# Kernel optimization log

Hardware: AMD Instinct MI355X
Metric: run time of the kernel (lower is better)

## Reference

```python
import jax, jax.numpy as jnp
import numpy as np

B, CIN, COUT, H, W = 16, 128, 128, 64, 64
E, PS, FF = 8, 16, 8
GC, HID, HC = 4 * FF, 64, COUT * 4  # gate_channel, gate hidden, bottleneck hidden


def conv(x, w, stride=1, pad=0, groups=1):
    # x: [B,C,H,W], w: [O,I/groups,kh,kw]
    return jax.lax.conv_general_dilated(
        x, w, (stride, stride), [(pad, pad), (pad, pad)], feature_group_count=groups)


def group_norm(x, scale, bias, groups, eps=1e-5):
    b, c = x.shape[:2]
    xr = x.reshape(b, groups, c // groups, *x.shape[2:])
    m = xr.mean(axis=(2, 3, 4), keepdims=True)
    v = xr.var(axis=(2, 3, 4), keepdims=True)
    xr = (xr - m) * jax.lax.rsqrt(v + eps)
    return xr.reshape(x.shape) * scale[None, :, None, None] + bias[None, :, None, None]


def setup_inputs() -> dict:
    key = jax.random.key(0)
    ks = jax.random.split(key, 8)
    f = lambda k, shp: jax.random.normal(k, shp, jnp.float32) * 0.05
    return dict(
        x=jax.random.normal(ks[0], (B, CIN, H, W), jnp.float32),
        w_exp=f(ks[1], (E, COUT, CIN, 3, 3)),
        gn_exp_s=jnp.ones((E, COUT), jnp.float32),
        gn_exp_b=jnp.zeros((E, COUT), jnp.float32),
        w1=f(ks[2], (GC, HID)), b1=jnp.zeros((HID,), jnp.float32),
        w2=f(ks[3], (HID, E)), b2=jnp.zeros((E,), jnp.float32),
        w_pw1=f(ks[4], (HC, COUT, 1, 1)),
        gn1_s=jnp.ones((HC,), jnp.float32), gn1_b=jnp.zeros((HC,), jnp.float32),
        w_dw=f(ks[5], (HC, 1, 3, 3)),
        gn2_s=jnp.ones((HC,), jnp.float32), gn2_b=jnp.zeros((HC,), jnp.float32),
        w_pw2=f(ks[6], (COUT, HC, 1, 1)),
        gn3_s=jnp.ones((COUT,), jnp.float32), gn3_b=jnp.zeros((COUT,), jnp.float32),
    )


def reference(x, w_exp, gn_exp_s, gn_exp_b, w1, b1, w2, b2,
              w_pw1, gn1_s, gn1_b, w_dw, gn2_s, gn2_b, w_pw2, gn3_s, gn3_b):
    # ---- Conv experts (residual 3x3 conv + GN + SiLU), vmapped over experts ----
    def expert(w, s, b):
        y = conv(x, w, pad=1)
        y = group_norm(y, s, b, groups=min(8, COUT))
        return jax.nn.silu(y) + x  # use_residual=True, CIN == COUT

    ys = jax.vmap(expert)(w_exp, gn_exp_s, gn_exp_b)  # [E,B,C,H,W]

    # ---- Router gate: Fourier features of patch-center coordinates ----
    ph, pw = H // PS, W // PS
    cy = (jnp.arange(ph, dtype=jnp.float32) + 0.5) / ph
    cx = (jnp.arange(pw, dtype=jnp.float32) + 0.5) / pw
    freqs = (2.0 ** jnp.arange(FF, dtype=jnp.float32)) * jnp.pi
    ay = cy[:, None] * freqs  # [ph,FF]
    ax = cx[:, None] * freqs  # [pw,FF]
    feats = jnp.concatenate([
        jnp.broadcast_to(jnp.sin(ay)[:, None, :], (ph, pw, FF)),
        jnp.broadcast_to(jnp.cos(ay)[:, None, :], (ph, pw, FF)),
        jnp.broadcast_to(jnp.sin(ax)[None, :, :], (ph, pw, FF)),
        jnp.broadcast_to(jnp.cos(ax)[None, :, :], (ph, pw, FF)),
    ], axis=-1)  # [ph,pw,4*FF] == gate_channel
    hgate = jax.nn.silu(feats @ w1 + b1)
    wts = jax.nn.softmax(hgate @ w2 + b2, axis=-1)  # [ph,pw,E]

    # ---- Patch-wise combine of expert outputs ----
    wmap = jnp.repeat(jnp.repeat(wts, PS, axis=0), PS, axis=1)  # [H,W,E]
    combined = jnp.einsum('ebchw,hwe->bchw', ys, wmap)

    # ---- Inverted bottleneck: 1x1 -> dw3x3 -> 1x1(stride2) with GN+SiLU ----
    h = jax.nn.silu(group_norm(conv(combined, w_pw1), gn1_s, gn1_b, groups=8))
    h = jax.nn.silu(group_norm(conv(h, w_dw, pad=1, groups=HC), gn2_s, gn2_b, groups=8))
    h = jax.nn.silu(group_norm(conv(h, w_pw2, stride=2), gn3_s, gn3_b, groups=8))
    return h  # [B, COUT, H//2, W//2]
```

## Files before the change

### kernel.cpp

```cpp
#include <hip/hip_runtime.h>
#include <hip/hip_bf16.h>


#define B_ 16
#define CIN_ 128
#define COUT_ 128
#define H_ 64
#define W_ 64
#define HW_ 4096
#define E_ 8
#define FF_ 8
#define GC_ 32
#define HID_ 64
#define HC_ 512

typedef __hip_bfloat16 bf16;
typedef __bf16 bf16x8 __attribute__((ext_vector_type(8)));
typedef float f32x4 __attribute__((ext_vector_type(4)));
typedef float f32x16 __attribute__((ext_vector_type(16)));

__device__ __forceinline__ float siluf(float v) {
  return v * __builtin_amdgcn_rcpf(1.f + __expf(-v));
}
__device__ __forceinline__ float bf2f(bf16 v) { return __bfloat162float(v); }
__device__ __forceinline__ bf16 f2bf(float v) { return __float2bfloat16(v); }

__device__ __forceinline__ void async16(void* lds, const void* g) {
  __builtin_amdgcn_global_load_lds(
      (const __attribute__((address_space(1))) unsigned int*)g,
      (__attribute__((address_space(3))) unsigned int*)lds, 16, 0, 0);
}

__global__ __launch_bounds__(256) void prep_kernel(
    const float* __restrict__ x, bf16* __restrict__ xT,
    const float* __restrict__ w_exp, bf16* __restrict__ wT,
    const float* __restrict__ w_pw1, const float* __restrict__ w_pw2,
    bf16* __restrict__ wp1T, bf16* __restrict__ wp2T,
    const float* __restrict__ w1, const float* __restrict__ b1,
    const float* __restrict__ w2, const float* __restrict__ b2,
    float* __restrict__ wts) {
  __shared__ float t[128][65];
  int blk = blockIdx.x;
  int tid = threadIdx.x;

  if (blk < 1024) {
    int b = blk >> 6, h = blk & 63;
    int w = tid & 63, c4 = tid >> 6;
    const float* xb = x + ((size_t)(b * 128) * 64 + h) * 64;
#pragma unroll 4
    for (int rep = 0; rep < 32; ++rep) {
      int ci = rep * 4 + c4;
      t[ci][w] = xb[(size_t)ci * HW_ + w];
    }
    __syncthreads();
    bf16* dst = xT + (size_t)(b * 64 + h) * 8192;
#pragma unroll 4
    for (int rep = 0; rep < 32; ++rep) {
      int o = rep * 256 + tid;
      int cg = o >> 9, w2 = (o >> 3) & 63, lo = o & 7;
      dst[o] = f2bf(t[cg * 8 + lo][w2]);
    }
  } else if (blk < 5632) {
    int idx = (blk - 1024) * 256 + tid;
    if (idx < 1179648) {
      int lo = idx & 7;
      int co = (idx >> 3) & 127;
      int cg = (idx >> 10) & 15;
      int rest = idx >> 14;
      int tap = rest % 9, e = rest / 9;
      int ci = cg * 8 + lo;
      wT[idx] = f2bf(w_exp[(((size_t)(e * 128 + co) * 128 + ci) * 9) + tap]);
    }
  } else if (blk < 6144) {
    int idx = (blk - 5632) * 256 + tid;
    if (idx < 65536) wp1T[idx] = f2bf(w_pw1[idx]);
    else wp2T[idx - 65536] = f2bf(w_pw2[idx - 65536]);
  } else {
    int p = tid;
    if (p >= 16) return;
    int i = p >> 2, j = p & 3;
    float cy = (i + 0.5f) * 0.25f;
    float cx = (j + 0.5f) * 0.25f;
    float feats[GC_];
#pragma unroll
    for (int f = 0; f < FF_; ++f) {
      float fr = 3.14159265358979f * (float)(1 << f);
      float ay = cy * fr, ax = cx * fr;
      feats[f] = sinf(ay);
      feats[FF_ + f] = cosf(ay);
      feats[2 * FF_ + f] = sinf(ax);
      feats[3 * FF_ + f] = cosf(ax);
    }
    float hid[HID_];
    for (int k = 0; k < HID_; ++k) {
      float a = b1[k];
#pragma unroll
      for (int m = 0; m < GC_; ++m) a = fmaf(feats[m], w1[m * HID_ + k], a);
      hid[k] = siluf(a);
    }
    float lg[E_];
    float mx = -1e30f;
#pragma unroll
    for (int e = 0; e < E_; ++e) {
      float a = b2[e];
      for (int k = 0; k < HID_; ++k) a = fmaf(hid[k], w2[k * E_ + e], a);
      lg[e] = a;
      mx = fmaxf(mx, a);
    }
    float s = 0.f;
#pragma unroll
    for (int e = 0; e < E_; ++e) { lg[e] = __expf(lg[e] - mx); s += lg[e]; }
    float inv = 1.f / s;
#pragma unroll
    for (int e = 0; e < E_; ++e) wts[p * E_ + e] = lg[e] * inv;
  }
}

__global__ __launch_bounds__(256, 2) void conv_mfma(
    const bf16* __restrict__ xT, const bf16* __restrict__ wT,
    float* __restrict__ statsE, bf16* __restrict__ ys) {
  __shared__ __align__(16) char xls[4 * 6336];
  __shared__ __align__(16) char wls[2][3 * 8192];
  __shared__ float red[4][8][2];

  int blk = blockIdx.x;
  int xcd = blk & 7;
  int r2 = blk >> 3;
  int b = xcd * 2 + (r2 & 1);
  int rest = r2 >> 1;
  int rt = rest & 15, e = rest >> 4;

  int tid = threadIdx.x, lane = tid & 63, wave = tid >> 6;
  int hi = lane >> 5, l31 = lane & 31;
  int h0 = rt * 4;

  if (tid < 48) {
    int cg = tid / 12, rem = tid % 12;
    int r = rem >> 1, edge = rem & 1;
    *(uint4*)(xls + cg * 6336 + r * 1056 + edge * 1040) = make_uint4(0u, 0u, 0u, 0u);
  }
  int rbad = (rt == 0) ? 0 : (rt == 15 ? 5 : -1);
  if (rbad >= 0) {
    int cg = tid >> 6, slot = (tid & 63) + 1;
    *(uint4*)(xls + cg * 6336 + rbad * 1056 + slot * 16) = make_uint4(0u, 0u, 0u, 0u);
  }

  f32x16 acc[4][2];
#pragma unroll
  for (int mt = 0; mt < 4; ++mt)
#pragma unroll
    for (int nt = 0; nt < 2; ++nt)
#pragma unroll
      for (int r = 0; r < 16; ++r) acc[mt][nt][r] = 0.f;

  for (int q = 0; q < 4; ++q) {
    if (q) __syncthreads();
    {
      int cg = wave;
#pragma unroll
      for (int r = 0; r < 6; ++r) {
        int h = h0 - 1 + r;
        if ((unsigned)h < 64u) {
          const char* g = (const char*)xT +
              ((size_t)((b * 64 + h) * 16) + q * 4 + cg) * 1024 + lane * 16;
          async16(xls + cg * 6336 + r * 1056 + 16, g);
        }
      }
    }
#pragma unroll
    for (int s = 0; s < 6; ++s) {
      int seg = wave * 6 + s;
      int tap = seg >> 3, rem = seg & 7;
      int cg = rem >> 1, cb = rem & 1;
      const char* g = (const char*)wT +
          ((size_t)(((e * 9 + tap) * 16) + q * 4 + cg) * 128 + cb * 64) * 16 + lane * 16;
      async16(wls[0] + (tap * 4 + cg) * 2048 + cb * 1024, g);
    }
    __syncthreads();

    for (int dr = 0; dr < 3; ++dr) {
      int buf = dr & 1;
      if (dr < 2) {
#pragma unroll
        for (int s = 0; s < 6; ++s) {
          int seg = wave * 6 + s;
          int tap = seg >> 3, rem = seg & 7;
          int cg = rem >> 1, cb = rem & 1;
          const char* g = (const char*)wT +
              ((size_t)(((e * 9 + (dr + 1) * 3 + tap) * 16) + q * 4 + cg) * 128 + cb * 64) * 16 +
              lane * 16;
          async16(wls[buf ^ 1] + (tap * 4 + cg) * 2048 + cb * 1024, g);
        }
      }
      int r_local = wave + dr;
      const char* wb = wls[buf];
      const char* xrow = xls;
      bf16x8 afp[2][2], bfp[2][2];
      {
        int cgl = hi;
        afp[0][0] = *(const bf16x8*)(wb + cgl * 2048 + (0 * 32 + l31) * 16);
        afp[0][1] = *(const bf16x8*)(wb + cgl * 2048 + (1 * 32 + l31) * 16);
        const char* xr = xrow + cgl * 6336 + r_local * 1056;
        bfp[0][0] = *(const bf16x8*)(xr + (0 * 32 + l31 + 0) * 16);
        bfp[0][1] = *(const bf16x8*)(xr + (1 * 32 + l31 + 0) * 16);
      }
#pragma unroll
      for (int s = 0; s < 12; ++s) {
        int mh = s & 1;
        int cura = s & 1, curb = (s >> 1) & 1;
        if (s < 11) {
          int s1 = s + 1;
          int ds1 = s1 >> 2, ks1 = (s1 >> 1) & 1, mh1 = s1 & 1;
          int cgl1 = ks1 * 2 + hi;
          const char* wt1 = wb + ds1 * 8192 + cgl1 * 2048;
          afp[s1 & 1][0] = *(const bf16x8*)(wt1 + ((mh1 * 2 + 0) * 32 + l31) * 16);
          afp[s1 & 1][1] = *(const bf16x8*)(wt1 + ((mh1 * 2 + 1) * 32 + l31) * 16);
          if (mh1 == 0) {
            const char* xr1 = xrow + cgl1 * 6336 + r_local * 1056;
            bfp[(s1 >> 1) & 1][0] = *(const bf16x8*)(xr1 + (0 * 32 + l31 + ds1) * 16);
            bfp[(s1 >> 1) & 1][1] = *(const bf16x8*)(xr1 + (1 * 32 + l31 + ds1) * 16);
          }
        }
#pragma unroll
        for (int i = 0; i < 2; ++i)
#pragma unroll
          for (int nt = 0; nt < 2; ++nt)
            acc[mh * 2 + i][nt] = __builtin_amdgcn_mfma_f32_32x32x16_bf16(
                afp[cura][i], bfp[curb][nt], acc[mh * 2 + i][nt], 0, 0, 0);
      }
      if (dr < 2) __syncthreads();
    }
  }

  int hh = h0 + wave;
  bf16* yb = ys + (size_t)((e * 16 + b) * 128) * 4096;
#pragma unroll
  for (int mt = 0; mt < 4; ++mt) {
    float s0 = 0.f, ss0 = 0.f, s1 = 0.f, ss1 = 0.f;
#pragma unroll
    for (int nt = 0; nt < 2; ++nt) {
      int w = nt * 32 + l31;
      int pos = hh * 64 + w;
#pragma unroll
      for (int r = 0; r < 16; ++r) {
        float v = acc[mt][nt][r];
        if (r < 8) { s0 += v; ss0 += v * v; } else { s1 += v; ss1 += v * v; }
        int row = (r & 3) + 8 * (r >> 2) + 4 * hi;
        yb[(size_t)(mt * 32 + row) * 4096 + pos] = f2bf(v);
      }
    }
#pragma unroll
    for (int off = 32; off; off >>= 1) {
      s0 += __shfl_down(s0, off, 64);
      ss0 += __shfl_down(ss0, off, 64);
      s1 += __shfl_down(s1, off, 64);
      ss1 += __shfl_down(ss1, off, 64);
    }
    if (lane == 0) {
      red[wave][mt * 2][0] = s0; red[wave][mt * 2][1] = ss0;
      red[wave][mt * 2 + 1][0] = s1; red[wave][mt * 2 + 1][1] = ss1;
    }
  }
  __syncthreads();
  if (tid < 16) {
    int g = tid >> 1, which = tid & 1;
    float t = red[0][g][which] + red[1][g][which] + red[2][g][which] + red[3][g][which];
    atomicAdd(&statsE[((e * 16 + b) * 8 + g) * 2 + which], t);
  }
}

__global__ __launch_bounds__(256) void combine_cl(
    const float* __restrict__ x, const bf16* __restrict__ ys,
    const float* __restrict__ stE, const float* __restrict__ gns,
    const float* __restrict__ gnb, const float* __restrict__ wts,
    bf16* __restrict__ ccl) {
  __shared__ bf16 tile[64][132];
  int blk = blockIdx.x;
  int xcd = blk & 7;
  int k2 = blk >> 3;
  int b = xcd * 2 + (k2 >> 6);
  int h = k2 & 63;
  int t = threadIdx.x;
  int oct = t & 7, cq = t >> 3;
  int w0 = oct * 8;
  int gidx = cq >> 2;
  int pid = (h >> 4) * 4 + (w0 >> 4);
  int pos = h * 64 + w0;

  float m_[8], r_[8], wt_[8];
#pragma unroll
  for (int e = 0; e < 8; ++e) {
    float S = stE[((e * 16 + b) * 8 + gidx) * 2];
    float SS = stE[((e * 16 + b) * 8 + gidx) * 2 + 1];
    float mean = S * (1.f / 65536.f);
    float var = SS * (1.f / 65536.f) - mean * mean;
    m_[e] = mean;
    r_[e] = rsqrtf(var + 1e-5f);
    wt_[e] = wts[pid * 8 + e];
  }

#pragma unroll
  for (int k = 0; k < 4; ++k) {
    int co = cq * 4 + k;
    const float* xp = x + ((size_t)(b * 128 + co) << 12) + pos;
    float v[8];
    float4 xa = *(const float4*)xp;
    float4 xb2 = *(const float4*)(xp + 4);
    v[0] = xa.x; v[1] = xa.y; v[2] = xa.z; v[3] = xa.w;
    v[4] = xb2.x; v[5] = xb2.y; v[6] = xb2.z; v[7] = xb2.w;
#pragma unroll
    for (int e = 0; e < 8; ++e) {
      uint4 u = *(const uint4*)(ys + ((size_t)((e * 16 + b) * 128 + co) << 12) + pos);
      const bf16* pv = (const bf16*)&u;
      float sc = r_[e] * gns[e * 128 + co];
      float sh = gnb[e * 128 + co] - m_[e] * sc;
#pragma unroll
      for (int j = 0; j < 8; ++j) {
        float yn = bf2f(pv[j]) * sc + sh;
        v[j] = fmaf(siluf(yn), wt_[e], v[j]);
      }
    }
#pragma unroll
    for (int j = 0; j < 8; ++j) tile[w0 + j][co] = f2bf(v[j]);
  }
  __syncthreads();
  int row = t >> 2, q = t & 3;
  char* dst = (char*)ccl + ((size_t)(b * 4096 + h * 64 + row)) * 256 + q * 64;
  const char* src = (const char*)&tile[row][0] + q * 64;
#pragma unroll
  for (int i = 0; i < 4; ++i)
    *(uint4*)(dst + i * 16) = *(const uint4*)(src + i * 16);
}

__global__ __launch_bounds__(256) void pw1_mfma(
    const bf16* __restrict__ ccl, const bf16* __restrict__ wp1T,
    bf16* __restrict__ h1cl, float* __restrict__ stats1) {
  __shared__ __align__(16) char bls[32768];
  __shared__ __align__(16) char ls2[34816];
  __shared__ float red[4][2][2];
  int blk = blockIdx.x;
  int n0 = blk * 128;
  int t = threadIdx.x, lane = t & 63, wave = t >> 6;
  int quad = lane >> 4, l15 = lane & 15;
  int b = n0 >> 12;

#pragma unroll
  for (int i = 0; i < 8; ++i) {
    int id = t + 256 * i;
    int r = id >> 4, c = id & 15;
    *(uint4*)(bls + c * 2048 + r * 16) =
        *(const uint4*)((const char*)ccl + (size_t)(n0 + r) * 256 + c * 16);
  }

  for (int mtile = 0; mtile < 4; ++mtile) {
    int m0 = mtile * 128;
    char* als = ls2;
#pragma unroll
    for (int i = 0; i < 8; ++i) {
      int id = t + 256 * i;
      int r = id >> 4, c = id & 15;
      *(uint4*)(als + c * 2048 + r * 16) =
          *(const uint4*)((const char*)wp1T + (size_t)(m0 + r) * 256 + c * 16);
    }
    __syncthreads();

    f32x4 acc[8][2];
#pragma unroll
    for (int mt = 0; mt < 8; ++mt)
#pragma unroll
      for (int nt = 0; nt < 2; ++nt) acc[mt][nt] = (f32x4){0.f, 0.f, 0.f, 0.f};

#pragma unroll
    for (int kc = 0; kc < 4; ++kc) {
      int cgq = kc * 4 + quad;
      bf16x8 af[8];
#pragma unroll
      for (int mt = 0; mt < 8; ++mt)
        af[mt] = *(const bf16x8*)(als + cgq * 2048 + (mt * 16 + l15) * 16);
      bf16x8 bfr[2];
#pragma unroll
      for (int nt = 0; nt < 2; ++nt)
        bfr[nt] = *(const bf16x8*)(bls + cgq * 2048 + (wave * 32 + nt * 16 + l15) * 16);
#pragma unroll
      for (int mt = 0; mt < 8; ++mt)
#pragma unroll
        for (int nt = 0; nt < 2; ++nt)
          acc[mt][nt] = __builtin_amdgcn_mfma_f32_16x16x32_bf16(
              af[mt], bfr[nt], acc[mt][nt], 0, 0, 0);
    }

    __syncthreads();
    float s[2] = {0.f, 0.f}, ss[2] = {0.f, 0.f};
    bf16* tile = (bf16*)ls2;
#pragma unroll
    for (int mt = 0; mt < 8; ++mt) {
      int gi = mt >> 2;
#pragma unroll
      for (int nt = 0; nt < 2; ++nt) {
        int n = wave * 32 + nt * 16 + l15;
#pragma unroll
        for (int r = 0; r < 4; ++r) {
          float v = acc[mt][nt][r];
          s[gi] += v;
          ss[gi] += v * v;
          tile[n * 132 + mt * 16 + quad * 4 + r] = f2bf(v);
        }
      }
    }
#pragma unroll
    for (int gi = 0; gi < 2; ++gi) {
#pragma unroll
      for (int off = 32; off; off >>= 1) {
        s[gi] += __shfl_down(s[gi], off, 64);
        ss[gi] += __shfl_down(ss[gi], off, 64);
      }
    }
    if (lane == 0) {
      red[wave][0][0] = s[0]; red[wave][0][1] = ss[0];
      red[wave][1][0] = s[1]; red[wave][1][1] = ss[1];
    }
    __syncthreads();
    if (t < 4) {
      int gi = t >> 1, which = t & 1;
      float v = red[0][gi][which] + red[1][gi][which] + red[2][gi][which] + red[3][gi][which];
      atomicAdd(&stats1[(b * 8 + mtile * 2 + gi) * 2 + which], v);
    }
#pragma unroll
    for (int i = 0; i < 8; ++i) {
      int id = t + 256 * i;
      int r = id >> 4, q = id & 15;
      char* dst = (char*)h1cl + (size_t)(n0 + r) * 1024 + m0 * 2 + q * 16;
      const char* src = (const char*)tile + r * 264 + q * 16;
      *(uint4*)dst = *(const uint4*)src;
    }
    __syncthreads();
  }
}

__global__ __launch_bounds__(256) void dw_cl(
    const bf16* __restrict__ h1cl, const float* __restrict__ w_dw,
    const float* __restrict__ st1, const float* __restrict__ gs,
    const float* __restrict__ gb, bf16* __restrict__ h2cl,
    float* __restrict__ stats2) {
  __shared__ __align__(16) bf16 tile[18 * 66 * 16];
  __shared__ float red2[4][2];
  int blk = blockIdx.x;
  int ht = blk & 3, hcg = (blk >> 2) & 31, b = blk >> 7;
  int h0 = ht * 16;
  int hc0 = hcg * 16;
  int hcb = hcg >> 2;
  int t = threadIdx.x;

  float S1 = st1[(b * 8 + hcb) * 2], SS1 = st1[(b * 8 + hcb) * 2 + 1];
  float mean = S1 * (1.f / 262144.f);
  float var1 = SS1 * (1.f / 262144.f) - mean * mean;
  float rstd = rsqrtf(var1 + 1e-5f);
  float scale[16], shift[16];
#pragma unroll
  for (int j = 0; j < 16; ++j) {
    float g = gs[hc0 + j];
    scale[j] = rstd * g;
    shift[j] = gb[hc0 + j] - mean * rstd * g;
  }

  for (int i = 0; i < 5; ++i) {
    int idx = t + 256 * i;
    if (idx >= 1188) break;
    int row = idx / 66, wslot = idx - row * 66;
    int hh = h0 - 1 + row;
    int w = wslot - 1;
    int swz = (wslot >> 2) & 3;
    bf16* dst = tile + (row * 66 + wslot) * 16;
    if ((unsigned)hh < 64u && (unsigned)w < 64u) {
      const char* p = (const char*)h1cl + ((size_t)(b * 4096 + hh * 64 + w) * 512 + hc0) * 2;
      uint4 a0 = *(const uint4*)p;
      uint4 a1 = *(const uint4*)(p + 16);
      const bf16* pv = (const bf16*)&a0;
      const bf16* pv1 = (const bf16*)&a1;
      bf16 outv[16];
#pragma unroll
      for (int j = 0; j < 8; ++j)
        outv[j] = f2bf(siluf(bf2f(pv[j]) * scale[j] + shift[j]));
#pragma unroll
      for (int j = 0; j < 8; ++j)
        outv[8 + j] = f2bf(siluf(bf2f(pv1[j]) * scale[8 + j] + shift[8 + j]));
#pragma unroll
      for (int qq = 0; qq < 4; ++qq) {
        int ph = (qq + swz) & 3;
        *(uint2*)(dst + ph * 4) = *(const uint2*)(outv + qq * 4);
      }
    } else {
      *(uint4*)dst = make_uint4(0u, 0u, 0u, 0u);
      *(uint4*)(dst + 8) = make_uint4(0u, 0u, 0u, 0u);
    }
  }
  __syncthreads();

  int w = t & 63, q = t >> 6;
  float wv[9][4];
#pragma unroll
  for (int j = 0; j < 4; ++j) {
    int hc = hc0 + q * 4 + j;
#pragma unroll
    for (int tap = 0; tap < 9; ++tap) wv[tap][j] = w_dw[hc * 9 + tap];
  }

  f32x4 win[3][3];
  float acc_s = 0.f, acc_ss = 0.f;

  auto ld4 = [&](int r, int dwi) -> f32x4 {
    int slot = w + dwi;
    int ph = (q + (slot >> 2)) & 3;
    const bf16* p = tile + (r * 66 + slot) * 16 + ph * 4;
    uint2 u = *(const uint2*)p;
    const bf16* pb = (const bf16*)&u;
    return (f32x4){bf2f(pb[0]), bf2f(pb[1]), bf2f(pb[2]), bf2f(pb[3])};
  };

#pragma unroll
  for (int dwi = 0; dwi < 3; ++dwi) {
    win[0][dwi] = ld4(0, dwi);
    win[1][dwi] = ld4(1, dwi);
  }
#pragma unroll
  for (int orow = 0; orow < 16; ++orow) {
    int rnew = orow + 2;
    int ringn = rnew % 3;
#pragma unroll
    for (int dwi = 0; dwi < 3; ++dwi) win[ringn][dwi] = ld4(rnew, dwi);
    f32x4 acc = (f32x4){0.f, 0.f, 0.f, 0.f};
#pragma unroll
    for (int dr = 0; dr < 3; ++dr) {
      int ring = (orow + dr) % 3;
#pragma unroll
      for (int dwi = 0; dwi < 3; ++dwi) {
#pragma unroll
        for (int j = 0; j < 4; ++j)
          acc[j] = fmaf(win[ring][dwi][j], wv[dr * 3 + dwi][j], acc[j]);
      }
    }
#pragma unroll
    for (int j = 0; j < 4; ++j) { acc_s += acc[j]; acc_ss += acc[j] * acc[j]; }
    if (!(orow & 1) && !(w & 1)) {
      int hglob = h0 + orow;
      int pos2 = (hglob >> 1) * 32 + (w >> 1);
      bf16 tmp[4];
#pragma unroll
      for (int j = 0; j < 4; ++j) tmp[j] = f2bf(acc[j]);
      *(uint2*)((char*)h2cl + ((size_t)(b * 1024 + pos2) * 512 + hc0 + q * 4) * 2) =
          *(const uint2*)tmp;
    }
  }

#pragma unroll
  for (int off = 32; off; off >>= 1) {
    acc_s += __shfl_down(acc_s, off, 64);
    acc_ss += __shfl_down(acc_ss, off, 64);
  }
  int wave = t >> 6;
  if ((t & 63) == 0) { red2[wave][0] = acc_s; red2[wave][1] = acc_ss; }
  __syncthreads();
  if (t < 2) {
    float v = red2[0][t] + red2[1][t] + red2[2][t] + red2[3][t];
    atomicAdd(&stats2[(b * 8 + hcb) * 2 + t], v);
  }
}

__global__ __launch_bounds__(256) void pw2_mfma(
    const bf16* __restrict__ h2, const bf16* __restrict__ wp2T,
    const float* __restrict__ st2, const float* __restrict__ gs2,
    const float* __restrict__ gb2, float* __restrict__ h3,
    float* __restrict__ stats3) {
  __shared__ __align__(16) char als[2][8192];
  __shared__ __align__(16) char bls[2][4096];
  __shared__ float red[4][8][2];
  int blk = blockIdx.x;
  int n0 = blk * 64;
  int b = n0 >> 10, posb = n0 & 1023;
  int t = threadIdx.x, lane = t & 63, wave = t >> 6;
  int quad = lane >> 4, l15 = lane & 15;
  int wbase = wave * 16;
  int c4 = t >> 6, r = t & 63;

  auto load_bls = [&](char* dst, int kc) {
    int hc0 = (kc * 4 + c4) * 8;
    int g = hc0 >> 6;
    float S = st2[(b * 8 + g) * 2], SS = st2[(b * 8 + g) * 2 + 1];
    float mean = S * (1.f / 262144.f);
    float rstd = rsqrtf(SS * (1.f / 262144.f) - mean * mean + 1e-5f);
    uint4 u = *(const uint4*)((const char*)h2 + (size_t)(n0 + r) * 1024 +
                              (size_t)(kc * 4 + c4) * 16);
    const bf16* pv = (const bf16*)&u;
    bf16 outv[8];
#pragma unroll
    for (int j = 0; j < 8; ++j) {
      float xv = bf2f(pv[j]);
      xv = (xv - mean) * rstd * gs2[hc0 + j] + gb2[hc0 + j];
      outv[j] = f2bf(siluf(xv));
    }
    *(uint4*)dst = *(const uint4*)outv;
  };

  f32x4 acc[8];
#pragma unroll
  for (int mt = 0; mt < 8; ++mt) acc[mt] = (f32x4){0.f, 0.f, 0.f, 0.f};

  {
#pragma unroll
    for (int i = 0; i < 2; ++i) {
      int id = t + 256 * i;
      int cc = id >> 7, rr = id & 127;
      *(uint4*)(als[0] + cc * 2048 + rr * 16) =
          *(const uint4*)((const char*)wp2T + (size_t)rr * 1024 + cc * 16);
    }
    load_bls(bls[0] + c4 * 1024 + r * 16, 0);
  }
#pragma unroll
  for (int kc = 0; kc < 16; ++kc) {
    __syncthreads();
    if (kc + 1 < 16) {
      int nb = (kc + 1) & 1;
#pragma unroll
      for (int i = 0; i < 2; ++i) {
        int id = t + 256 * i;
        int cc = id >> 7, rr = id & 127;
        *(uint4*)(als[nb] + cc * 2048 + rr * 16) =
            *(const uint4*)((const char*)wp2T + (size_t)rr * 1024 + ((kc + 1) * 4 + cc) * 16);
      }
      load_bls(bls[nb] + c4 * 1024 + r * 16, kc + 1);
    }
    int buf = kc & 1;
    bf16x8 bf1 = *(const bf16x8*)(bls[buf] + quad * 1024 + (wbase + l15) * 16);
#pragma unroll
    for (int mt = 0; mt < 8; ++mt) {
      bf16x8 af = *(const bf16x8*)(als[buf] + quad * 2048 + (mt * 16 + l15) * 16);
      acc[mt] = __builtin_amdgcn_mfma_f32_16x16x32_bf16(af, bf1, acc[mt], 0, 0, 0);
    }
  }

#pragma unroll
  for (int mt = 0; mt < 8; ++mt) {
    float s = 0.f, ss = 0.f;
    int pos = posb + wbase + l15;
#pragma unroll
    for (int rr = 0; rr < 4; ++rr) {
      float v = acc[mt][rr];
      s += v;
      ss += v * v;
      int co = mt * 16 + quad * 4 + rr;
      h3[(size_t)(b * 128 + co) * 1024 + pos] = v;
    }
#pragma unroll
    for (int off = 32; off; off >>= 1) {
      s += __shfl_down(s, off, 64);
      ss += __shfl_down(ss, off, 64);
    }
    if (lane == 0) { red[wave][mt][0] = s; red[wave][mt][1] = ss; }
  }
  __syncthreads();
  if (t < 16) {
    int mt = t >> 1, which = t & 1;
    float v = red[0][mt][which] + red[1][mt][which] + red[2][mt][which] + red[3][mt][which];
    atomicAdd(&stats3[(b * 8 + mt) * 2 + which], v);
  }
}

__global__ void out_kernel(const float* __restrict__ h3, const float* __restrict__ stats,
                           const float* __restrict__ gs, const float* __restrict__ gb,
                           float* __restrict__ out) {
  const int total4 = (B_ * COUT_ * 1024) >> 2;
  for (int i4 = blockIdx.x * blockDim.x + threadIdx.x; i4 < total4;
       i4 += gridDim.x * blockDim.x) {
    int idx = i4 << 2;
    int c = (idx >> 10) & 127;
    int b = idx >> 17;
    int bg = b * 8 + (c >> 4);
    float S = stats[bg * 2], SS = stats[bg * 2 + 1];
    float mean = S * (1.f / 16384.f);
    float var = SS * (1.f / 16384.f) - mean * mean;
    float rstd = rsqrtf(var + 1e-5f);
    float sc = rstd * gs[c];
    float sh = gb[c] - mean * sc;
    float4 hv = *(const float4*)(h3 + idx);
    float4 res;
    res.x = siluf(hv.x * sc + sh);
    res.y = siluf(hv.y * sc + sh);
    res.z = siluf(hv.z * sc + sh);
    res.w = siluf(hv.w * sc + sh);
    *(float4*)(out + idx) = res;
  }
}

extern "C" void kernel_launch(void* const* d_in, const int* in_sizes, int n_in,
                              void* d_out, int out_size, void* d_ws, size_t ws_size,
                              hipStream_t stream) {
  const float* x = (const float*)d_in[0];
  const float* w_exp = (const float*)d_in[1];
  const float* gn_exp_s = (const float*)d_in[2];
  const float* gn_exp_b = (const float*)d_in[3];
  const float* w1 = (const float*)d_in[4];
  const float* b1 = (const float*)d_in[5];
  const float* w2 = (const float*)d_in[6];
  const float* b2 = (const float*)d_in[7];
  const float* w_pw1 = (const float*)d_in[8];
  const float* gn1_s = (const float*)d_in[9];
  const float* gn1_b = (const float*)d_in[10];
  const float* w_dw = (const float*)d_in[11];
  const float* gn2_s = (const float*)d_in[12];
  const float* gn2_b = (const float*)d_in[13];
  const float* w_pw2 = (const float*)d_in[14];
  const float* gn3_s = (const float*)d_in[15];
  const float* gn3_b = (const float*)d_in[16];

  char* ws = (char*)d_ws;
  const size_t WP1T_OFF = 16384;
  const size_t WP2T_OFF = WP1T_OFF + 131072;
  const size_t XT_OFF = WP2T_OFF + 131072;
  const size_t WT_OFF = XT_OFF + 16777216;
  const size_t YS_OFF = WT_OFF + 2359296;
  const size_t NEEDED = YS_OFF + 134217728;
  if (ws_size < NEEDED) return;

  float* wts = (float*)ws;
  float* stats1 = (float*)(ws + 1024);
  float* stats2 = (float*)(ws + 2048);
  float* stats3 = (float*)(ws + 3072);
  float* statsE = (float*)(ws + 4096);
  bf16* wp1T = (bf16*)(ws + WP1T_OFF);
  bf16* wp2T = (bf16*)(ws + WP2T_OFF);
  bf16* xT = (bf16*)(ws + XT_OFF);
  bf16* ccl = (bf16*)(ws + XT_OFF);
  bf16* wT = (bf16*)(ws + WT_OFF);
  bf16* ys = (bf16*)(ws + YS_OFF);
  bf16* h1cl = (bf16*)(ws + YS_OFF);
  bf16* h2cl = (bf16*)(ws + YS_OFF + 67108864);
  float* h3 = (float*)(ws + YS_OFF + 83886080);

  hipMemsetAsync(ws, 0, 16384, stream);
  prep_kernel<<<6145, 256, 0, stream>>>(x, xT, w_exp, wT, w_pw1, w_pw2, wp1T, wp2T,
                                        w1, b1, w2, b2, wts);
  conv_mfma<<<E_ * B_ * 16, 256, 0, stream>>>(xT, wT, statsE, ys);
  combine_cl<<<B_ * 64, 256, 0, stream>>>(x, ys, statsE, gn_exp_s, gn_exp_b, wts, ccl);
  pw1_mfma<<<512, 256, 0, stream>>>(ccl, wp1T, h1cl, stats1);
  dw_cl<<<B_ * 32 * 4, 256, 0, stream>>>(h1cl, w_dw, stats1, gn1_s, gn1_b, h2cl, stats2);
  pw2_mfma<<<256, 256, 0, stream>>>(h2cl, wp2T, stats2, gn2_s, gn2_b, h3, stats3);
  out_kernel<<<1024, 256, 0, stream>>>(h3, stats3, gn3_s, gn3_b, (float*)d_out);
}
```

Before: 437.6 us.

## Split conv and pw2 launches, fold stats memset into prep kernel

Removes the hipMemsetAsync by zeroing the stats region inside prep_kernel's last block. Splits the expert conv launch into two launches of four experts each via an e_base offset. Splits pw2_mfma over output-channel halves, doubling the grid to 512 blocks with half the accumulators and smaller LDS per block. The pw2 split gains occupancy and parallelism but recomputes the GN2+SiLU B-tile in both halves. The conv split adds a launch boundary with no clear benefit.

New measurement: 432.9 us. About the same (-1.1%).

```diff
diff --git a/kernel.cpp b/kernel.cpp
--- a/kernel.cpp
+++ b/kernel.cpp
@@ -76,6 +76,8 @@
     if (idx < 65536) wp1T[idx] = f2bf(w_pw1[idx]);
     else wp2T[idx - 65536] = f2bf(w_pw2[idx - 65536]);
   } else {
+    uint4* z = (uint4*)((char*)wts + 1024);
+    for (int i = tid; i < 960; i += 256) z[i] = make_uint4(0u, 0u, 0u, 0u);
     int p = tid;
     if (p >= 16) return;
     int i = p >> 2, j = p & 3;
@@ -118,7 +120,7 @@
 
 __global__ __launch_bounds__(256, 2) void conv_mfma(
     const bf16* __restrict__ xT, const bf16* __restrict__ wT,
-    float* __restrict__ statsE, bf16* __restrict__ ys) {
+    float* __restrict__ statsE, bf16* __restrict__ ys, int e_base) {
   __shared__ __align__(16) char xls[4 * 6336];
   __shared__ __align__(16) char wls[2][3 * 8192];
   __shared__ float red[4][8][2];
@@ -128,7 +130,7 @@
   int r2 = blk >> 3;
   int b = xcd * 2 + (r2 & 1);
   int rest = r2 >> 1;
-  int rt = rest & 15, e = rest >> 4;
+  int rt = rest & 15, e = e_base + (rest >> 4);
 
   int tid = threadIdx.x, lane = tid & 63, wave = tid >> 6;
   int hi = lane >> 5, l31 = lane & 31;
@@ -571,11 +573,14 @@
     const float* __restrict__ st2, const float* __restrict__ gs2,
     const float* __restrict__ gb2, float* __restrict__ h3,
     float* __restrict__ stats3) {
-  __shared__ __align__(16) char als[2][8192];
+  __shared__ __align__(16) char als[2][4096];
   __shared__ __align__(16) char bls[2][4096];
-  __shared__ float red[4][8][2];
+  __shared__ float red[4][4][2];
   int blk = blockIdx.x;
-  int n0 = blk * 64;
+  int mhalf = blk >> 8;
+  int nblk = blk & 255;
+  int n0 = nblk * 64;
+  int m0 = mhalf * 64;
   int b = n0 >> 10, posb = n0 & 1023;
   int t = threadIdx.x, lane = t & 63, wave = t >> 6;
   int quad = lane >> 4, l15 = lane & 15;
@@ -600,19 +605,18 @@
     }
     *(uint4*)dst = *(const uint4*)outv;
   };
-
-  f32x4 acc[8];
-#pragma unroll
-  for (int mt = 0; mt < 8; ++mt) acc[mt] = (f32x4){0.f, 0.f, 0.f, 0.f};
+  auto load_als = [&](char* dstbase, int kc) {
+    *(uint4*)(dstbase + c4 * 1024 + r * 16) =
+        *(const uint4*)((const char*)wp2T + (size_t)(m0 + r) * 1024 +
+                        (size_t)(kc * 4 + c4) * 16);
+  };
+
+  f32x4 acc[4];
+#pragma unroll
+  for (int mt = 0; mt < 4; ++mt) acc[mt] = (f32x4){0.f, 0.f, 0.f, 0.f};
 
   {
-#pragma unroll
-    for (int i = 0; i < 2; ++i) {
-      int id = t + 256 * i;
-      int cc = id >> 7, rr = id & 127;
-      *(uint4*)(als[0] + cc * 2048 + rr * 16) =
-          *(const uint4*)((const char*)wp2T + (size_t)rr * 1024 + cc * 16);
-    }
+    load_als(als[0], 0);
     load_bls(bls[0] + c4 * 1024 + r * 16, 0);
   }
 #pragma unroll
@@ -620,26 +624,20 @@
     __syncthreads();
     if (kc + 1 < 16) {
       int nb = (kc + 1) & 1;
-#pragma unroll
-      for (int i = 0; i < 2; ++i) {
-        int id = t + 256 * i;
-        int cc = id >> 7, rr = id & 127;
-        *(uint4*)(als[nb] + cc * 2048 + rr * 16) =
-            *(const uint4*)((const char*)wp2T + (size_t)rr * 1024 + ((kc + 1) * 4 + cc) * 16);
-      }
+      load_als(als[nb], kc + 1);
       load_bls(bls[nb] + c4 * 1024 + r * 16, kc + 1);
     }
     int buf = kc & 1;
     bf16x8 bf1 = *(const bf16x8*)(bls[buf] + quad * 1024 + (wbase + l15) * 16);
 #pragma unroll
-    for (int mt = 0; mt < 8; ++mt) {
-      bf16x8 af = *(const bf16x8*)(als[buf] + quad * 2048 + (mt * 16 + l15) * 16);
+    for (int mt = 0; mt < 4; ++mt) {
+      bf16x8 af = *(const bf16x8*)(als[buf] + quad * 1024 + (mt * 16 + l15) * 16);
       acc[mt] = __builtin_amdgcn_mfma_f32_16x16x32_bf16(af, bf1, acc[mt], 0, 0, 0);
     }
   }
 
 #pragma unroll
-  for (int mt = 0; mt < 8; ++mt) {
+  for (int mt = 0; mt < 4; ++mt) {
     float s = 0.f, ss = 0.f;
     int pos = posb + wbase + l15;
 #pragma unroll
@@ -647,7 +645,7 @@
       float v = acc[mt][rr];
       s += v;
       ss += v * v;
-      int co = mt * 16 + quad * 4 + rr;
+      int co = m0 + mt * 16 + quad * 4 + rr;
       h3[(size_t)(b * 128 + co) * 1024 + pos] = v;
     }
 #pragma unroll
@@ -658,10 +656,10 @@
     if (lane == 0) { red[wave][mt][0] = s; red[wave][mt][1] = ss; }
   }
   __syncthreads();
-  if (t < 16) {
+  if (t < 8) {
     int mt = t >> 1, which = t & 1;
     float v = red[0][mt][which] + red[1][mt][which] + red[2][mt][which] + red[3][mt][which];
-    atomicAdd(&stats3[(b * 8 + mt) * 2 + which], v);
+    atomicAdd(&stats3[(b * 8 + mhalf * 4 + mt) * 2 + which], v);
   }
 }
 
@@ -736,13 +734,13 @@
   bf16* h2cl = (bf16*)(ws + YS_OFF + 67108864);
   float* h3 = (float*)(ws + YS_OFF + 83886080);
 
-  hipMemsetAsync(ws, 0, 16384, stream);
   prep_kernel<<<6145, 256, 0, stream>>>(x, xT, w_exp, wT, w_pw1, w_pw2, wp1T, wp2T,
                                         w1, b1, w2, b2, wts);
-  conv_mfma<<<E_ * B_ * 16, 256, 0, stream>>>(xT, wT, statsE, ys);
+  conv_mfma<<<1024, 256, 0, stream>>>(xT, wT, statsE, ys, 0);
+  conv_mfma<<<1024, 256, 0, stream>>>(xT, wT, statsE, ys, 4);
   combine_cl<<<B_ * 64, 256, 0, stream>>>(x, ys, statsE, gn_exp_s, gn_exp_b, wts, ccl);
   pw1_mfma<<<512, 256, 0, stream>>>(ccl, wp1T, h1cl, stats1);
   dw_cl<<<B_ * 32 * 4, 256, 0, stream>>>(h1cl, w_dw, stats1, gn1_s, gn1_b, h2cl, stats2);
-  pw2_mfma<<<256, 256, 0, stream>>>(h2cl, wp2T, stats2, gn2_s, gn2_b, h3, stats3);
+  pw2_mfma<<<512, 256, 0, stream>>>(h2cl, wp2T, stats2, gn2_s, gn2_b, h3, stats3);
   out_kernel<<<1024, 256, 0, stream>>>(h3, stats3, gn3_s, gn3_b, (float*)d_out);
 }
```
